# Performance work log

Hardware: AMD Instinct MI355X
Metric: run time of the kernel (lower is better)

## Reference

```python
import jax, jax.numpy as jnp
import numpy as np

DEPTH = 4
EPS = 1e-5


def block_pool(x, g):
    # adaptive max pool over a g x g grid of blocks, broadcast back to full size.
    # Equivalent to the recursive HalfSplit/adaptive_max_pool2d/QuarterStitch pyramid.
    B, C, H, W = x.shape
    xr = x.reshape(B, C, g, H // g, g, W // g)
    m = xr.max(axis=(3, 5), keepdims=True)          # [B,C,g,1,g,1]
    return jnp.broadcast_to(m, xr.shape).reshape(B, C, H, W)


def conv1x1_bn(x, w, gamma, beta):
    # Conv2DNormed: 1x1 conv (no bias) followed by BatchNorm (batch statistics).
    y = jnp.einsum('bchw,oc->bohw', x, w)
    mu = y.mean(axis=(0, 2, 3), keepdims=True)
    var = y.var(axis=(0, 2, 3), keepdims=True)
    yhat = (y - mu) * jax.lax.rsqrt(var + EPS)
    return yhat * gamma[None, :, None, None] + beta[None, :, None, None]


def setup_inputs() -> dict:
    key = jax.random.key(0)
    k0, k1, k2 = jax.random.split(key, 3)
    B, C, H, W = 4, 256, 192, 192
    x = jax.random.normal(k0, (B, C, H, W), jnp.float32)
    ws = jax.random.normal(k1, (DEPTH, C, C), jnp.float32) / np.float32(np.sqrt(C))
    gs = jnp.ones((DEPTH, C), jnp.float32)
    bs = jnp.zeros((DEPTH, C), jnp.float32)
    wf = jax.random.normal(k2, (C, (DEPTH + 1) * C), jnp.float32) / np.float32(np.sqrt((DEPTH + 1) * C))
    gf = jnp.ones((C,), jnp.float32)
    bf = jnp.zeros((C,), jnp.float32)
    return {"x": x, "ws": ws, "gs": gs, "bs": bs, "wf": wf, "gf": gf, "bf": bf}


def reference(x, ws, gs, bs, wf, gf, bf):
    # p[0] = raw input; p[1+d] = conv_d(block-pooled input at grid 2^d), d=0..DEPTH-1
    p = [x]
    for d in range(DEPTH):
        pooled = block_pool(x, 2 ** d)
        p.append(conv1x1_bn(pooled, ws[d], gs[d], bs[d]))
    out = jnp.concatenate(p, axis=1)                # [B, (DEPTH+1)*C, H, W]
    return conv1x1_bn(out, wf, gf, bf)
```

## Files before the change

### kernel.cpp

```cpp
#include <hip/hip_runtime.h>

typedef unsigned short u16;
typedef unsigned int   u32;
typedef __attribute__((ext_vector_type(4))) float f32x4;
typedef __attribute__((ext_vector_type(8))) short s16x8;
typedef __attribute__((ext_vector_type(4))) unsigned short u16x4;

#define HW    36864
#define WPIX  192
#define NCH   256
#define NB    4
#define NPIX  147456
#define POS   85
#define BN_EPS 1e-5f
#define NBKT  16

#define WS_PALL    0
#define WS_YD      (WS_PALL + NB*NCH*POS)
#define WS_PSUM    (WS_YD + NB*NCH*POS)
#define WS_PSQ     (WS_PSUM + 1024)
#define WS_PSC     (WS_PSQ + 1024)
#define WS_PBI     (WS_PSC + 1024)
#define WS_CONTRIB (WS_PBI + 1024)
#define WS_FSUMB   (WS_CONTRIB + NB*NCH*64)
#define WS_FSQB    (WS_FSUMB + NBKT*256)
#define WS_FSC     (WS_FSQB + NBKT*256)
#define WS_FBI     (WS_FSC + 256)
#define WS_WPK     (WS_FBI + 256)
#define WS_YBF     (WS_WPK + 32768)
#define WS_YBF_FLOATS (NB*NCH*HW/2)
#define WS_TOTAL   (WS_YBF + WS_YBF_FLOATS)

__device__ __forceinline__ u16 f2bf(float f) {
  u32 u = __builtin_bit_cast(u32, f);
  u += 0x7fffu + ((u >> 16) & 1u);
  return (u16)(u >> 16);
}
__device__ __forceinline__ float bf2f(u16 h) {
  u32 u = ((u32)h) << 16;
  return __builtin_bit_cast(float, u);
}

__global__ __launch_bounds__(192) void k_pool(const float* __restrict__ x, float* __restrict__ wsb) {
  __shared__ float sm[8][4][48];
  __shared__ float sp[84];
  int bc = blockIdx.x;
  const float* base = x + (size_t)bc * HW;
  int t = threadIdx.x;
  int cg = t % 48, rg = t / 48;
  if (bc == 0) {
    for (int i = t; i < 2048; i += 192) wsb[WS_PSUM + i] = 0.f;
    for (int i = t; i < 2*NBKT*256; i += 192) wsb[WS_FSUMB + i] = 0.f;
  }
  #pragma unroll
  for (int byi = 0; byi < 8; byi++) {
    float mm = -3.4e38f;
    #pragma unroll
    for (int rr = 0; rr < 6; rr++) {
      int r = byi*24 + rg + 4*rr;
      f32x4 v = *(const f32x4*)(base + r*WPIX + cg*4);
      mm = fmaxf(mm, fmaxf(fmaxf(v.x, v.y), fmaxf(v.z, v.w)));
    }
    sm[byi][rg][cg] = mm;
  }
  __syncthreads();
  size_t pb = WS_PALL + (size_t)bc * POS;
  if (t < 64) {
    int by = t >> 3, bx = t & 7;
    float mm = -3.4e38f;
    for (int r2 = 0; r2 < 4; r2++)
      for (int cq = 0; cq < 6; cq++)
        mm = fmaxf(mm, sm[by][r2][bx*6 + cq]);
    sp[t] = mm;
    wsb[pb + t] = mm;
  }
  __syncthreads();
  if (t < 16) {
    int i = t >> 2, j = t & 3;
    float mm = fmaxf(fmaxf(sp[(2*i)*8 + 2*j], sp[(2*i)*8 + 2*j + 1]),
                     fmaxf(sp[(2*i+1)*8 + 2*j], sp[(2*i+1)*8 + 2*j + 1]));
    sp[64 + t] = mm;
    wsb[pb + 64 + t] = mm;
  }
  __syncthreads();
  if (t < 4) {
    int i = t >> 1, j = t & 1;
    float mm = fmaxf(fmaxf(sp[64 + (2*i)*4 + 2*j], sp[64 + (2*i)*4 + 2*j + 1]),
                     fmaxf(sp[64 + (2*i+1)*4 + 2*j], sp[64 + (2*i+1)*4 + 2*j + 1]));
    sp[80 + t] = mm;
    wsb[pb + 80 + t] = mm;
  }
  __syncthreads();
  if (t == 0)
    wsb[pb + 84] = fmaxf(fmaxf(sp[80], sp[81]), fmaxf(sp[82], sp[83]));
}

__global__ __launch_bounds__(256) void k_wpack(const float* __restrict__ wf, float* __restrict__ wsb) {
  int fid = blockIdx.x*256 + threadIdx.x;
  int m = fid & 255, g = (fid >> 8) & 3, ks = fid >> 10;
  const float* src = wf + (size_t)m*1280 + ks*32 + g*8;
  f32x4 a = *(const f32x4*)src;
  f32x4 c = *(const f32x4*)(src + 4);
  u32* dst = (u32*)((u16*)(wsb + WS_WPK) + (size_t)fid*8);
  dst[0] = (u32)f2bf(a.x) | ((u32)f2bf(a.y) << 16);
  dst[1] = (u32)f2bf(a.z) | ((u32)f2bf(a.w) << 16);
  dst[2] = (u32)f2bf(c.x) | ((u32)f2bf(c.y) << 16);
  dst[3] = (u32)f2bf(c.z) | ((u32)f2bf(c.w) << 16);
}

__global__ __launch_bounds__(256) void k_pyr(const float* __restrict__ wconv, float* __restrict__ wsb) {
  __shared__ __align__(16) float pv[256];
  int bi = blockIdx.x;
  int b = bi / 85, pos = bi % 85;
  int d = (pos < 64) ? 3 : (pos < 80) ? 2 : (pos < 84) ? 1 : 0;
  int t = threadIdx.x;
  pv[t] = wsb[WS_PALL + (size_t)(b*NCH + t)*POS + pos];
  __syncthreads();
  const float* wrow = wconv + ((size_t)d*NCH + t)*NCH;
  float acc = 0.f;
  #pragma unroll 4
  for (int c4 = 0; c4 < 64; c4++) {
    f32x4 wv = *(const f32x4*)(wrow + c4*4);
    f32x4 xv = *(const f32x4*)(&pv[c4*4]);
    acc += wv.x*xv.x + wv.y*xv.y + wv.z*xv.z + wv.w*xv.w;
  }
  wsb[WS_YD + (size_t)(b*NCH + t)*POS + pos] = acc;
  atomicAdd(&wsb[WS_PSUM + d*NCH + t], acc);
  atomicAdd(&wsb[WS_PSQ  + d*NCH + t], acc*acc);
}

__global__ void k_pstats(const float* __restrict__ gs, const float* __restrict__ bs, float* __restrict__ wsb) {
  int t = blockIdx.x*256 + threadIdx.x;
  int d = t >> 8;
  float cnt = (float)(4 << (2*d));
  float mu  = wsb[WS_PSUM + t] / cnt;
  float var = wsb[WS_PSQ + t] / cnt - mu*mu;
  float sc  = gs[t] * rsqrtf(var + BN_EPS);
  wsb[WS_PSC + t] = sc;
  wsb[WS_PBI + t] = bs[t] - mu * sc;
}

__global__ __launch_bounds__(256) void k_contrib(const float* __restrict__ wf, float* __restrict__ wsb) {
  __shared__ __align__(16) float pn[1024];
  int bi = blockIdx.x;
  int b = bi >> 6, cell = bi & 63;
  int by = cell >> 3, bx = cell & 7;
  int t = threadIdx.x;
  int pos3 = cell;
  int pos2 = 64 + (by >> 1)*4 + (bx >> 1);
  int pos1 = 80 + (by >> 2)*2 + (bx >> 2);
  size_t yb = WS_YD + (size_t)(b*NCH + t)*POS;
  pn[0*NCH + t] = wsb[yb + 84]   * wsb[WS_PSC + 0*NCH + t] + wsb[WS_PBI + 0*NCH + t];
  pn[1*NCH + t] = wsb[yb + pos1] * wsb[WS_PSC + 1*NCH + t] + wsb[WS_PBI + 1*NCH + t];
  pn[2*NCH + t] = wsb[yb + pos2] * wsb[WS_PSC + 2*NCH + t] + wsb[WS_PBI + 2*NCH + t];
  pn[3*NCH + t] = wsb[yb + pos3] * wsb[WS_PSC + 3*NCH + t] + wsb[WS_PBI + 3*NCH + t];
  __syncthreads();
  const float* wrow = wf + (size_t)t*1280 + 256;
  float acc = 0.f;
  #pragma unroll 4
  for (int j = 0; j < 256; j++) {
    f32x4 wv = *(const f32x4*)(wrow + j*4);
    f32x4 xv = *(const f32x4*)(&pn[j*4]);
    acc += wv.x*xv.x + wv.y*xv.y + wv.z*xv.z + wv.w*xv.w;
  }
  wsb[WS_CONTRIB + (size_t)(b*NCH + t)*64 + cell] = acc;
}

template<bool YBF>
__global__ __launch_bounds__(256) void k_main(const float* __restrict__ x,
                                              float* __restrict__ wsb, float* __restrict__ y) {
  __shared__ __align__(16) u16 xlds[2][64*40];
  int wg = blockIdx.x;
  int b = wg / 576, nt = wg % 576;
  int pbase = nt * 64;
  int by8   = ((nt / 3) / 24) * 8;
  int wbase = (nt % 3) * 64;
  int t = threadIdx.x;
  int wave = t >> 6, l = t & 63;
  int g = l >> 4, ln = l & 15;
  int sn = t & 63;
  int kh = t >> 6;
  const float* xb = x + (size_t)b*NCH*HW + pbase + sn;
  const u16* wpk = (const u16*)(wsb + WS_WPK);
  int mrow = wave*64 + ln;

  f32x4 acc[4][4];
  #pragma unroll
  for (int i = 0; i < 4; i++)
    #pragma unroll
    for (int j = 0; j < 4; j++)
      acc[i][j] = {0.f, 0.f, 0.f, 0.f};

  float xr0[8], xr1[8];
  s16x8 a0[4], a1[4];

  #pragma unroll
  for (int j = 0; j < 8; j++) xr0[j] = xb[(size_t)(kh*8 + j)*HW];
  #pragma unroll
  for (int tm = 0; tm < 4; tm++)
    a0[tm] = *(const s16x8*)(wpk + ((size_t)(0*4 + g)*256 + mrow + tm*16)*8);

  #pragma unroll
  for (int ks = 0; ks < 8; ks++) {
    float    (&xr)[8] = (ks & 1) ? xr1 : xr0;
    s16x8    (&af)[4] = (ks & 1) ? a1  : a0;
    float    (&xrn)[8] = (ks & 1) ? xr0 : xr1;
    s16x8    (&afn)[4] = (ks & 1) ? a0  : a1;
    s16x8 pk;
    #pragma unroll
    for (int j = 0; j < 8; j++) pk[j] = (short)f2bf(xr[j]);
    *(s16x8*)(&xlds[ks & 1][sn*40 + kh*8]) = pk;
    __syncthreads();
    if (ks < 7) {
      #pragma unroll
      for (int j = 0; j < 8; j++) xrn[j] = xb[(size_t)((ks+1)*32 + kh*8 + j)*HW];
      #pragma unroll
      for (int tm = 0; tm < 4; tm++)
        afn[tm] = *(const s16x8*)(wpk + ((size_t)((ks+1)*4 + g)*256 + mrow + tm*16)*8);
    }
    #pragma unroll
    for (int tn = 0; tn < 4; tn++) {
      s16x8 bfr = *(const s16x8*)(&xlds[ks & 1][(tn*16 + ln)*40 + g*8]);
      #pragma unroll
      for (int tm = 0; tm < 4; tm++)
        acc[tm][tn] = __builtin_amdgcn_mfma_f32_16x16x32_bf16(af[tm], bfr, acc[tm][tn], 0, 0, 0);
    }
  }

  const float* cb = wsb + WS_CONTRIB + (size_t)b*NCH*64;
  int bkt = wg & (NBKT - 1);
  float* fsum = wsb + WS_FSUMB + bkt*256;
  float* fsq  = wsb + WS_FSQB  + bkt*256;
  u16*   ybb  = (u16*)(wsb + WS_YBF) + (size_t)b*NCH*HW + pbase;
  float* ybf32 = y + (size_t)b*NCH*HW + pbase;
  #pragma unroll
  for (int tm = 0; tm < 4; tm++) {
    int ob = wave*64 + tm*16 + g*4;
    #pragma unroll
    for (int r = 0; r < 4; r++) {
      int o = ob + r;
      float s1 = 0.f, s2 = 0.f;
      #pragma unroll
      for (int tn = 0; tn < 4; tn++) {
        int n = tn*16 + ln;
        int bx = (wbase + n) / 24;
        float yv = acc[tm][tn][r] + cb[(size_t)o*64 + by8 + bx];
        if (YBF) {
          u16 h = f2bf(yv);
          float yr = bf2f(h);
          ybb[(size_t)o*HW + n] = h;
          s1 += yr; s2 += yr*yr;
        } else {
          ybf32[(size_t)o*HW + n] = yv;
          s1 += yv; s2 += yv*yv;
        }
      }
      s1 += __shfl_xor(s1, 1);  s2 += __shfl_xor(s2, 1);
      s1 += __shfl_xor(s1, 2);  s2 += __shfl_xor(s2, 2);
      s1 += __shfl_xor(s1, 4);  s2 += __shfl_xor(s2, 4);
      s1 += __shfl_xor(s1, 8);  s2 += __shfl_xor(s2, 8);
      if (ln == 0) { atomicAdd(&fsum[o], s1); atomicAdd(&fsq[o], s2); }
    }
  }
}

__global__ void k_fstats(const float* __restrict__ gf, const float* __restrict__ bfv, float* __restrict__ wsb) {
  int o = threadIdx.x;
  float s1 = 0.f, s2 = 0.f;
  #pragma unroll
  for (int i = 0; i < NBKT; i++) {
    s1 += wsb[WS_FSUMB + i*256 + o];
    s2 += wsb[WS_FSQB  + i*256 + o];
  }
  float inv = 1.f / (float)NPIX;
  float mu  = s1 * inv;
  float var = s2 * inv - mu*mu;
  float sc  = gf[o] * rsqrtf(var + BN_EPS);
  wsb[WS_FSC + o] = sc;
  wsb[WS_FBI + o] = bfv[o] - mu * sc;
}

template<bool YBF>
__global__ __launch_bounds__(256) void k_norm(float* __restrict__ out, const float* __restrict__ wsb) {
  int bid = blockIdx.x;
  int plane = bid >> 2, q = bid & 3;
  int c = plane & 255;
  float sc = wsb[WS_FSC + c], bi = wsb[WS_FBI + c];
  size_t base4 = ((size_t)plane*HW + q*(HW/4)) >> 2;
  int t = threadIdx.x;
  if (YBF) {
    const u16* yb = (const u16*)(wsb + WS_YBF);
    #pragma unroll
    for (int it = 0; it < 9; it++) {
      size_t i4 = base4 + it*256 + t;
      u16x4 v = *(const u16x4*)(yb + i4*4);
      f32x4 o;
      o.x = bf2f(v.x)*sc + bi;
      o.y = bf2f(v.y)*sc + bi;
      o.z = bf2f(v.z)*sc + bi;
      o.w = bf2f(v.w)*sc + bi;
      ((f32x4*)out)[i4] = o;
    }
  } else {
    #pragma unroll
    for (int it = 0; it < 9; it++) {
      size_t i4 = base4 + it*256 + t;
      f32x4 v = ((f32x4*)out)[i4];
      v.x = v.x*sc + bi; v.y = v.y*sc + bi; v.z = v.z*sc + bi; v.w = v.w*sc + bi;
      ((f32x4*)out)[i4] = v;
    }
  }
}

extern "C" void kernel_launch(void* const* d_in, const int* in_sizes, int n_in,
                              void* d_out, int out_size, void* d_ws, size_t ws_size,
                              hipStream_t stream) {
  const float* x  = (const float*)d_in[0];
  const float* w  = (const float*)d_in[1];
  const float* gs = (const float*)d_in[2];
  const float* bs = (const float*)d_in[3];
  const float* wf = (const float*)d_in[4];
  const float* gf = (const float*)d_in[5];
  const float* bf = (const float*)d_in[6];
  float* y   = (float*)d_out;
  float* wsb = (float*)d_ws;

  bool ybf = ws_size >= (size_t)WS_TOTAL * sizeof(float);

  k_pool   <<<NB*NCH, 192, 0, stream>>>(x, wsb);
  k_wpack  <<<32, 256, 0, stream>>>(wf, wsb);
  k_pyr    <<<NB*POS, 256, 0, stream>>>(w, wsb);
  k_pstats <<<4, 256, 0, stream>>>(gs, bs, wsb);
  k_contrib<<<NB*64, 256, 0, stream>>>(wf, wsb);
  if (ybf) k_main<true> <<<NB*576, 256, 0, stream>>>(x, wsb, y);
  else     k_main<false><<<NB*576, 256, 0, stream>>>(x, wsb, y);
  k_fstats <<<1, 256, 0, stream>>>(gf, bf, wsb);
  if (ybf) k_norm<true> <<<4096, 256, 0, stream>>>(y, wsb);
  else     k_norm<false><<<4096, 256, 0, stream>>>(y, wsb);
}
```

Before: 200.4 us.

## Pre-transpose input to bf16 pixel-major layout and stream GEMM tiles via global_load_lds

Adds a prep kernel that converts the input once to a bf16 pixel-major, XOR-swizzled layout while computing row maxima, so the main GEMM loads its B tiles straight into LDS with global_load_lds and no per-tile conversion. The main kernel now covers 128 pixels per workgroup, with larger accumulator tiles and a min-blocks launch bound. Small kernels are merged: weight packing goes into prep, pyramid stats are folded into contrib (now split by depth and accumulated with atomics), and final stats are folded into the normalize kernel. The cost is an extra bf16 copy of the input (write then read) and more workspace, which the ybf path now requires.

```diff
diff --git a/kernel.cpp b/kernel.cpp
--- a/kernel.cpp
+++ b/kernel.cpp
@@ -4,10 +4,10 @@
 typedef unsigned int   u32;
 typedef __attribute__((ext_vector_type(4))) float f32x4;
 typedef __attribute__((ext_vector_type(8))) short s16x8;
+typedef __attribute__((ext_vector_type(4))) short s16x4;
 typedef __attribute__((ext_vector_type(4))) unsigned short u16x4;
 
 #define HW    36864
-#define WPIX  192
 #define NCH   256
 #define NB    4
 #define NPIX  147456
@@ -16,20 +16,18 @@
 #define NBKT  16
 
 #define WS_PALL    0
-#define WS_YD      (WS_PALL + NB*NCH*POS)
-#define WS_PSUM    (WS_YD + NB*NCH*POS)
-#define WS_PSQ     (WS_PSUM + 1024)
-#define WS_PSC     (WS_PSQ + 1024)
-#define WS_PBI     (WS_PSC + 1024)
-#define WS_CONTRIB (WS_PBI + 1024)
-#define WS_FSUMB   (WS_CONTRIB + NB*NCH*64)
-#define WS_FSQB    (WS_FSUMB + NBKT*256)
-#define WS_FSC     (WS_FSQB + NBKT*256)
-#define WS_FBI     (WS_FSC + 256)
-#define WS_WPK     (WS_FBI + 256)
-#define WS_YBF     (WS_WPK + 32768)
-#define WS_YBF_FLOATS (NB*NCH*HW/2)
-#define WS_TOTAL   (WS_YBF + WS_YBF_FLOATS)
+#define WS_YD      87040
+#define WS_PSUM    174080
+#define WS_PSQ     175104
+#define WS_CONTRIB 176128
+#define WS_FSUMB   241664
+#define WS_FSQB    245760
+#define WS_RM      249856
+#define WS_WPK     1822720
+#define WS_XT      1855488
+#define WS_YBF     20729856
+#define WS_TOT1    39604224
+#define WS_TOT2    20729856
 
 __device__ __forceinline__ u16 f2bf(float f) {
   u32 u = __builtin_bit_cast(u32, f);
@@ -40,72 +38,122 @@
   u32 u = ((u32)h) << 16;
   return __builtin_bit_cast(float, u);
 }
-
-__global__ __launch_bounds__(192) void k_pool(const float* __restrict__ x, float* __restrict__ wsb) {
-  __shared__ float sm[8][4][48];
-  __shared__ float sp[84];
+__device__ __forceinline__ void gl_lds16(const void* g, void* l) {
+  __builtin_amdgcn_global_load_lds(
+      (const __attribute__((address_space(1))) u32*)g,
+      (__attribute__((address_space(3))) u32*)l, 16, 0, 0);
+}
+
+#define LP 204
+
+__global__ __launch_bounds__(256) void k_prep(const float* __restrict__ x,
+                                              const float* __restrict__ wf,
+                                              float* __restrict__ wsb) {
+  int blk = blockIdx.x;
+  int t = threadIdx.x;
+  if (blk >= 768) {
+    int fid = (blk - 768)*256 + t;
+    int m = fid & 255, g = (fid >> 8) & 3, ks = fid >> 10;
+    const float* src = wf + (size_t)m*1280 + ks*32 + g*8;
+    f32x4 a = *(const f32x4*)src;
+    f32x4 c = *(const f32x4*)(src + 4);
+    u32* dst = (u32*)((u16*)(wsb + WS_WPK) + (size_t)fid*8);
+    dst[0] = (u32)f2bf(a.x) | ((u32)f2bf(a.y) << 16);
+    dst[1] = (u32)f2bf(a.z) | ((u32)f2bf(a.w) << 16);
+    dst[2] = (u32)f2bf(c.x) | ((u32)f2bf(c.y) << 16);
+    dst[3] = (u32)f2bf(c.z) | ((u32)f2bf(c.w) << 16);
+    if (blk == 768) {
+      for (int i = t; i < 2048;  i += 256) wsb[WS_PSUM + i] = 0.f;
+      for (int i = t; i < 65536; i += 256) wsb[WS_CONTRIB + i] = 0.f;
+      for (int i = t; i < 8192;  i += 256) wsb[WS_FSUMB + i] = 0.f;
+    }
+    return;
+  }
+  __shared__ u16 ldsT[32 * LP];
+  int b = blk / 192, r = blk % 192;
+  int c_l = t >> 3, grp = t & 7;
+  int px_w = t >> 2, oct_w = t & 3;
+  u16* xTu = (u16*)(wsb + WS_XT);
+  float* rm = wsb + WS_RM;
+  int p_row = r * 192;
+
+  for (int cc = 0; cc < 8; cc++) {
+    int c = cc*32 + c_l;
+    const float* src = x + (size_t)(b*NCH + c)*HW + p_row + grp*24;
+    float mm = -3.4e38f;
+    #pragma unroll
+    for (int q = 0; q < 6; q++) {
+      f32x4 v = *(const f32x4*)(src + q*4);
+      mm = fmaxf(mm, fmaxf(fmaxf(v.x, v.y), fmaxf(v.z, v.w)));
+      s16x4 pk;
+      pk[0] = (short)f2bf(v.x); pk[1] = (short)f2bf(v.y);
+      pk[2] = (short)f2bf(v.z); pk[3] = (short)f2bf(v.w);
+      *(s16x4*)&ldsT[c_l*LP + grp*24 + q*4] = pk;
+    }
+    rm[((size_t)(b*NCH + c)*192 + r)*8 + grp] = mm;
+    __syncthreads();
+    #pragma unroll
+    for (int i = 0; i < 3; i++) {
+      int px = i*64 + px_w;
+      s16x8 v;
+      #pragma unroll
+      for (int e = 0; e < 8; e++)
+        v[e] = (short)ldsT[(oct_w*8 + e)*LP + px];
+      int p_glob = p_row + px;
+      int slot = oct_w ^ ((px >> 1) & 3);
+      *(s16x8*)(xTu + ((size_t)b*HW + p_glob)*256 + cc*32 + slot*8) = v;
+    }
+    __syncthreads();
+  }
+}
+
+__global__ __launch_bounds__(64) void k_pmax(float* __restrict__ wsb) {
+  __shared__ float sm3[64], sm2[16], sm1[4], arr85[85];
   int bc = blockIdx.x;
-  const float* base = x + (size_t)bc * HW;
-  int t = threadIdx.x;
-  int cg = t % 48, rg = t / 48;
-  if (bc == 0) {
-    for (int i = t; i < 2048; i += 192) wsb[WS_PSUM + i] = 0.f;
-    for (int i = t; i < 2*NBKT*256; i += 192) wsb[WS_FSUMB + i] = 0.f;
-  }
-  #pragma unroll
-  for (int byi = 0; byi < 8; byi++) {
-    float mm = -3.4e38f;
-    #pragma unroll
-    for (int rr = 0; rr < 6; rr++) {
-      int r = byi*24 + rg + 4*rr;
-      f32x4 v = *(const f32x4*)(base + r*WPIX + cg*4);
-      mm = fmaxf(mm, fmaxf(fmaxf(v.x, v.y), fmaxf(v.z, v.w)));
-    }
-    sm[byi][rg][cg] = mm;
-  }
-  __syncthreads();
-  size_t pb = WS_PALL + (size_t)bc * POS;
-  if (t < 64) {
-    int by = t >> 3, bx = t & 7;
-    float mm = -3.4e38f;
-    for (int r2 = 0; r2 < 4; r2++)
-      for (int cq = 0; cq < 6; cq++)
-        mm = fmaxf(mm, sm[by][r2][bx*6 + cq]);
-    sp[t] = mm;
-    wsb[pb + t] = mm;
+  int t = threadIdx.x;
+  const float* rm = wsb + WS_RM + (size_t)bc*1536;
+  float v[24];
+  #pragma unroll
+  for (int q = 0; q < 6; q++)
+    *(f32x4*)&v[q*4] = *(const f32x4*)(rm + t*24 + q*4);
+  float m3p[8];
+  #pragma unroll
+  for (int j = 0; j < 8; j++)
+    m3p[j] = fmaxf(v[j], fmaxf(v[8+j], v[16+j]));
+  #pragma unroll
+  for (int j = 0; j < 8; j++) {
+    float m = m3p[j];
+    m = fmaxf(m, __shfl_xor(m, 1));
+    m = fmaxf(m, __shfl_xor(m, 2));
+    m = fmaxf(m, __shfl_xor(m, 4));
+    m3p[j] = m;
+  }
+  if ((t & 7) == 0) {
+    int br = t >> 3;
+    #pragma unroll
+    for (int j = 0; j < 8; j++) sm3[br*8 + j] = m3p[j];
   }
   __syncthreads();
   if (t < 16) {
     int i = t >> 2, j = t & 3;
-    float mm = fmaxf(fmaxf(sp[(2*i)*8 + 2*j], sp[(2*i)*8 + 2*j + 1]),
-                     fmaxf(sp[(2*i+1)*8 + 2*j], sp[(2*i+1)*8 + 2*j + 1]));
-    sp[64 + t] = mm;
-    wsb[pb + 64 + t] = mm;
+    sm2[t] = fmaxf(fmaxf(sm3[(2*i)*8 + 2*j], sm3[(2*i)*8 + 2*j + 1]),
+                   fmaxf(sm3[(2*i+1)*8 + 2*j], sm3[(2*i+1)*8 + 2*j + 1]));
   }
   __syncthreads();
   if (t < 4) {
     int i = t >> 1, j = t & 1;
-    float mm = fmaxf(fmaxf(sp[64 + (2*i)*4 + 2*j], sp[64 + (2*i)*4 + 2*j + 1]),
-                     fmaxf(sp[64 + (2*i+1)*4 + 2*j], sp[64 + (2*i+1)*4 + 2*j + 1]));
-    sp[80 + t] = mm;
-    wsb[pb + 80 + t] = mm;
-  }
-  __syncthreads();
-  if (t == 0)
-    wsb[pb + 84] = fmaxf(fmaxf(sp[80], sp[81]), fmaxf(sp[82], sp[83]));
-}
-
-__global__ __launch_bounds__(256) void k_wpack(const float* __restrict__ wf, float* __restrict__ wsb) {
-  int fid = blockIdx.x*256 + threadIdx.x;
-  int m = fid & 255, g = (fid >> 8) & 3, ks = fid >> 10;
-  const float* src = wf + (size_t)m*1280 + ks*32 + g*8;
-  f32x4 a = *(const f32x4*)src;
-  f32x4 c = *(const f32x4*)(src + 4);
-  u32* dst = (u32*)((u16*)(wsb + WS_WPK) + (size_t)fid*8);
-  dst[0] = (u32)f2bf(a.x) | ((u32)f2bf(a.y) << 16);
-  dst[1] = (u32)f2bf(a.z) | ((u32)f2bf(a.w) << 16);
-  dst[2] = (u32)f2bf(c.x) | ((u32)f2bf(c.y) << 16);
-  dst[3] = (u32)f2bf(c.z) | ((u32)f2bf(c.w) << 16);
+    sm1[t] = fmaxf(fmaxf(sm2[(2*i)*4 + 2*j], sm2[(2*i)*4 + 2*j + 1]),
+                   fmaxf(sm2[(2*i+1)*4 + 2*j], sm2[(2*i+1)*4 + 2*j + 1]));
+  }
+  __syncthreads();
+  if (t < 64) arr85[t] = sm3[t];
+  if (t < 16) arr85[64 + t] = sm2[t];
+  if (t < 4)  arr85[80 + t] = sm1[t];
+  if (t == 0) arr85[84] = fmaxf(fmaxf(sm1[0], sm1[1]), fmaxf(sm1[2], sm1[3]));
+  __syncthreads();
+  float* pb = wsb + WS_PALL + (size_t)bc*POS;
+  if (t < 85) pb[t] = arr85[t];
+  if (t >= 21 && t < 42) pb[t + 43] = arr85[t + 43];
 }
 
 __global__ __launch_bounds__(256) void k_pyr(const float* __restrict__ wconv, float* __restrict__ wsb) {
@@ -129,98 +177,93 @@
   atomicAdd(&wsb[WS_PSQ  + d*NCH + t], acc*acc);
 }
 
-__global__ void k_pstats(const float* __restrict__ gs, const float* __restrict__ bs, float* __restrict__ wsb) {
-  int t = blockIdx.x*256 + threadIdx.x;
-  int d = t >> 8;
+__global__ __launch_bounds__(256) void k_contrib(const float* __restrict__ wf,
+                                                 const float* __restrict__ gs,
+                                                 const float* __restrict__ bs,
+                                                 float* __restrict__ wsb) {
+  __shared__ __align__(16) float pn[4][256];
+  int bi = blockIdx.x;
+  int d = bi >> 6, cell = bi & 63;
+  int by = cell >> 3, bx = cell & 7;
+  int t = threadIdx.x;
+  int pos = (d == 3) ? cell
+          : (d == 2) ? 64 + (by >> 1)*4 + (bx >> 1)
+          : (d == 1) ? 80 + (by >> 2)*2 + (bx >> 2)
+          : 84;
   float cnt = (float)(4 << (2*d));
-  float mu  = wsb[WS_PSUM + t] / cnt;
-  float var = wsb[WS_PSQ + t] / cnt - mu*mu;
-  float sc  = gs[t] * rsqrtf(var + BN_EPS);
-  wsb[WS_PSC + t] = sc;
-  wsb[WS_PBI + t] = bs[t] - mu * sc;
-}
-
-__global__ __launch_bounds__(256) void k_contrib(const float* __restrict__ wf, float* __restrict__ wsb) {
-  __shared__ __align__(16) float pn[1024];
-  int bi = blockIdx.x;
-  int b = bi >> 6, cell = bi & 63;
-  int by = cell >> 3, bx = cell & 7;
-  int t = threadIdx.x;
-  int pos3 = cell;
-  int pos2 = 64 + (by >> 1)*4 + (bx >> 1);
-  int pos1 = 80 + (by >> 2)*2 + (bx >> 2);
-  size_t yb = WS_YD + (size_t)(b*NCH + t)*POS;
-  pn[0*NCH + t] = wsb[yb + 84]   * wsb[WS_PSC + 0*NCH + t] + wsb[WS_PBI + 0*NCH + t];
-  pn[1*NCH + t] = wsb[yb + pos1] * wsb[WS_PSC + 1*NCH + t] + wsb[WS_PBI + 1*NCH + t];
-  pn[2*NCH + t] = wsb[yb + pos2] * wsb[WS_PSC + 2*NCH + t] + wsb[WS_PBI + 2*NCH + t];
-  pn[3*NCH + t] = wsb[yb + pos3] * wsb[WS_PSC + 3*NCH + t] + wsb[WS_PBI + 3*NCH + t];
-  __syncthreads();
-  const float* wrow = wf + (size_t)t*1280 + 256;
-  float acc = 0.f;
+  float mu  = wsb[WS_PSUM + d*NCH + t] / cnt;
+  float var = wsb[WS_PSQ  + d*NCH + t] / cnt - mu*mu;
+  float sc  = gs[d*NCH + t] * rsqrtf(var + BN_EPS);
+  float bi_ = bs[d*NCH + t] - mu * sc;
+  #pragma unroll
+  for (int b = 0; b < 4; b++)
+    pn[b][t] = wsb[WS_YD + (size_t)(b*NCH + t)*POS + pos] * sc + bi_;
+  __syncthreads();
+  const float* wrow = wf + (size_t)t*1280 + 256 + d*256;
+  float a0 = 0.f, a1 = 0.f, a2 = 0.f, a3 = 0.f;
   #pragma unroll 4
-  for (int j = 0; j < 256; j++) {
+  for (int j = 0; j < 64; j++) {
     f32x4 wv = *(const f32x4*)(wrow + j*4);
-    f32x4 xv = *(const f32x4*)(&pn[j*4]);
-    acc += wv.x*xv.x + wv.y*xv.y + wv.z*xv.z + wv.w*xv.w;
-  }
-  wsb[WS_CONTRIB + (size_t)(b*NCH + t)*64 + cell] = acc;
+    f32x4 p0 = *(const f32x4*)(&pn[0][j*4]);
+    f32x4 p1 = *(const f32x4*)(&pn[1][j*4]);
+    f32x4 p2 = *(const f32x4*)(&pn[2][j*4]);
+    f32x4 p3 = *(const f32x4*)(&pn[3][j*4]);
+    a0 += wv.x*p0.x + wv.y*p0.y + wv.z*p0.z + wv.w*p0.w;
+    a1 += wv.x*p1.x + wv.y*p1.y + wv.z*p1.z + wv.w*p1.w;
+    a2 += wv.x*p2.x + wv.y*p2.y + wv.z*p2.z + wv.w*p2.w;
+    a3 += wv.x*p3.x + wv.y*p3.y + wv.z*p3.z + wv.w*p3.w;
+  }
+  atomicAdd(&wsb[WS_CONTRIB + (size_t)(0*NCH + t)*64 + cell], a0);
+  atomicAdd(&wsb[WS_CONTRIB + (size_t)(1*NCH + t)*64 + cell], a1);
+  atomicAdd(&wsb[WS_CONTRIB + (size_t)(2*NCH + t)*64 + cell], a2);
+  atomicAdd(&wsb[WS_CONTRIB + (size_t)(3*NCH + t)*64 + cell], a3);
 }
 
 template<bool YBF>
-__global__ __launch_bounds__(256) void k_main(const float* __restrict__ x,
-                                              float* __restrict__ wsb, float* __restrict__ y) {
-  __shared__ __align__(16) u16 xlds[2][64*40];
+__global__ __launch_bounds__(256, 3) void k_main(float* __restrict__ wsb, float* __restrict__ y) {
+  __shared__ __align__(16) u16 xlds[2][128*32];
   int wg = blockIdx.x;
-  int b = wg / 576, nt = wg % 576;
-  int pbase = nt * 64;
-  int by8   = ((nt / 3) / 24) * 8;
-  int wbase = (nt % 3) * 64;
+  int b = wg / 288, tile = wg % 288;
+  int n0 = tile * 128;
   int t = threadIdx.x;
   int wave = t >> 6, l = t & 63;
   int g = l >> 4, ln = l & 15;
-  int sn = t & 63;
-  int kh = t >> 6;
-  const float* xb = x + (size_t)b*NCH*HW + pbase + sn;
+  int spix = t >> 2, soct = t & 3;
+  const u16* xT = (const u16*)(wsb + WS_XT) + (size_t)b*HW*256;
   const u16* wpk = (const u16*)(wsb + WS_WPK);
-  int mrow = wave*64 + ln;
-
-  f32x4 acc[4][4];
+
+  f32x4 acc[4][8];
   #pragma unroll
   for (int i = 0; i < 4; i++)
     #pragma unroll
-    for (int j = 0; j < 4; j++)
+    for (int j = 0; j < 8; j++)
       acc[i][j] = {0.f, 0.f, 0.f, 0.f};
 
-  float xr0[8], xr1[8];
-  s16x8 a0[4], a1[4];
-
-  #pragma unroll
-  for (int j = 0; j < 8; j++) xr0[j] = xb[(size_t)(kh*8 + j)*HW];
-  #pragma unroll
-  for (int tm = 0; tm < 4; tm++)
-    a0[tm] = *(const s16x8*)(wpk + ((size_t)(0*4 + g)*256 + mrow + tm*16)*8);
-
+  {
+    const u16* s0 = xT + (size_t)(n0 + spix)*256 + soct*8;
+    gl_lds16(s0, &xlds[0][spix*32 + soct*8]);
+    gl_lds16(s0 + 64*256, &xlds[0][(64 + spix)*32 + soct*8]);
+  }
+
+  s16x8 af[4];
   #pragma unroll
   for (int ks = 0; ks < 8; ks++) {
-    float    (&xr)[8] = (ks & 1) ? xr1 : xr0;
-    s16x8    (&af)[4] = (ks & 1) ? a1  : a0;
-    float    (&xrn)[8] = (ks & 1) ? xr0 : xr1;
-    s16x8    (&afn)[4] = (ks & 1) ? a0  : a1;
-    s16x8 pk;
-    #pragma unroll
-    for (int j = 0; j < 8; j++) pk[j] = (short)f2bf(xr[j]);
-    *(s16x8*)(&xlds[ks & 1][sn*40 + kh*8]) = pk;
+    int abase = (ks*4 + g)*256 + wave*64 + ln;
+    #pragma unroll
+    for (int tm = 0; tm < 4; tm++)
+      af[tm] = *(const s16x8*)(wpk + (size_t)(abase + tm*16)*8);
     __syncthreads();
     if (ks < 7) {
-      #pragma unroll
-      for (int j = 0; j < 8; j++) xrn[j] = xb[(size_t)((ks+1)*32 + kh*8 + j)*HW];
-      #pragma unroll
-      for (int tm = 0; tm < 4; tm++)
-        afn[tm] = *(const s16x8*)(wpk + ((size_t)((ks+1)*4 + g)*256 + mrow + tm*16)*8);
-    }
-    #pragma unroll
-    for (int tn = 0; tn < 4; tn++) {
-      s16x8 bfr = *(const s16x8*)(&xlds[ks & 1][(tn*16 + ln)*40 + g*8]);
+      const u16* s0 = xT + (size_t)(n0 + spix)*256 + (ks + 1)*32 + soct*8;
+      u16* d0 = &xlds[(ks + 1) & 1][spix*32 + soct*8];
+      gl_lds16(s0, d0);
+      gl_lds16(s0 + 64*256, d0 + 64*32);
+    }
+    const u16* xb = xlds[ks & 1];
+    #pragma unroll
+    for (int tn = 0; tn < 8; tn++) {
+      int n = tn*16 + ln;
+      s16x8 bfr = *(const s16x8*)(xb + n*32 + ((g ^ ((n >> 1) & 3))*8));
       #pragma unroll
       for (int tm = 0; tm < 4; tm++)
         acc[tm][tn] = __builtin_amdgcn_mfma_f32_16x16x32_bf16(af[tm], bfr, acc[tm][tn], 0, 0, 0);
@@ -231,27 +274,30 @@
   int bkt = wg & (NBKT - 1);
   float* fsum = wsb + WS_FSUMB + bkt*256;
   float* fsq  = wsb + WS_FSQB  + bkt*256;
-  u16*   ybb  = (u16*)(wsb + WS_YBF) + (size_t)b*NCH*HW + pbase;
-  float* ybf32 = y + (size_t)b*NCH*HW + pbase;
+  u16*   ybb  = (u16*)(wsb + WS_YBF) + (size_t)b*NCH*HW + n0;
+  float* yf   = y + (size_t)b*NCH*HW + n0;
   #pragma unroll
   for (int tm = 0; tm < 4; tm++) {
     int ob = wave*64 + tm*16 + g*4;
     #pragma unroll
-    for (int r = 0; r < 4; r++) {
-      int o = ob + r;
+    for (int r_ = 0; r_ < 4; r_++) {
+      int o = ob + r_;
+      const float* cbo = cb + (size_t)o*64;
       float s1 = 0.f, s2 = 0.f;
       #pragma unroll
-      for (int tn = 0; tn < 4; tn++) {
+      for (int tn = 0; tn < 8; tn++) {
         int n = tn*16 + ln;
-        int bx = (wbase + n) / 24;
-        float yv = acc[tm][tn][r] + cb[(size_t)o*64 + by8 + bx];
+        u32 p = (u32)(n0 + n);
+        u32 row = p / 192u;
+        u32 col = p - row*192u;
+        float yv = acc[tm][tn][r_] + cbo[(row/24u)*8u + col/24u];
         if (YBF) {
           u16 h = f2bf(yv);
           float yr = bf2f(h);
           ybb[(size_t)o*HW + n] = h;
           s1 += yr; s2 += yr*yr;
         } else {
-          ybf32[(size_t)o*HW + n] = yv;
+          yf[(size_t)o*HW + n] = yv;
           s1 += yv; s2 += yv*yv;
         }
       }
@@ -264,28 +310,25 @@
   }
 }
 
-__global__ void k_fstats(const float* __restrict__ gf, const float* __restrict__ bfv, float* __restrict__ wsb) {
-  int o = threadIdx.x;
+template<bool YBF>
+__global__ __launch_bounds__(256) void k_norm(float* __restrict__ out,
+                                              const float* __restrict__ gf,
+                                              const float* __restrict__ bfv,
+                                              const float* __restrict__ wsb) {
+  int bid = blockIdx.x;
+  int plane = bid >> 2, q = bid & 3;
+  int c = plane & 255;
   float s1 = 0.f, s2 = 0.f;
   #pragma unroll
   for (int i = 0; i < NBKT; i++) {
-    s1 += wsb[WS_FSUMB + i*256 + o];
-    s2 += wsb[WS_FSQB  + i*256 + o];
+    s1 += wsb[WS_FSUMB + i*256 + c];
+    s2 += wsb[WS_FSQB  + i*256 + c];
   }
   float inv = 1.f / (float)NPIX;
   float mu  = s1 * inv;
   float var = s2 * inv - mu*mu;
-  float sc  = gf[o] * rsqrtf(var + BN_EPS);
-  wsb[WS_FSC + o] = sc;
-  wsb[WS_FBI + o] = bfv[o] - mu * sc;
-}
-
-template<bool YBF>
-__global__ __launch_bounds__(256) void k_norm(float* __restrict__ out, const float* __restrict__ wsb) {
-  int bid = blockIdx.x;
-  int plane = bid >> 2, q = bid & 3;
-  int c = plane & 255;
-  float sc = wsb[WS_FSC + c], bi = wsb[WS_FBI + c];
+  float sc  = gf[c] * rsqrtf(var + BN_EPS);
+  float bi  = bfv[c] - mu * sc;
   size_t base4 = ((size_t)plane*HW + q*(HW/4)) >> 2;
   int t = threadIdx.x;
   if (YBF) {
@@ -325,16 +368,14 @@
   float* y   = (float*)d_out;
   float* wsb = (float*)d_ws;
 
-  bool ybf = ws_size >= (size_t)WS_TOTAL * sizeof(float);
-
-  k_pool   <<<NB*NCH, 192, 0, stream>>>(x, wsb);
-  k_wpack  <<<32, 256, 0, stream>>>(wf, wsb);
+  bool ybf = ws_size >= (size_t)WS_TOT1 * sizeof(float);
+
+  k_prep   <<<800, 256, 0, stream>>>(x, wf, wsb);
+  k_pmax   <<<NB*NCH, 64, 0, stream>>>(wsb);
   k_pyr    <<<NB*POS, 256, 0, stream>>>(w, wsb);
-  k_pstats <<<4, 256, 0, stream>>>(gs, bs, wsb);
-  k_contrib<<<NB*64, 256, 0, stream>>>(wf, wsb);
-  if (ybf) k_main<true> <<<NB*576, 256, 0, stream>>>(x, wsb, y);
-  else     k_main<false><<<NB*576, 256, 0, stream>>>(x, wsb, y);
-  k_fstats <<<1, 256, 0, stream>>>(gf, bf, wsb);
-  if (ybf) k_norm<true> <<<4096, 256, 0, stream>>>(y, wsb);
-  else     k_norm<false><<<4096, 256, 0, stream>>>(y, wsb);
-}
+  k_contrib<<<256, 256, 0, stream>>>(wf, gs, bs, wsb);
+  if (ybf) k_main<true> <<<NB*288, 256, 0, stream>>>(wsb, y);
+  else     k_main<false><<<NB*288, 256, 0, stream>>>(wsb, y);
+  if (ybf) k_norm<true> <<<4096, 256, 0, stream>>>(y, gf, bf, wsb);
+  else     k_norm<false><<<4096, 256, 0, stream>>>(y, gf, bf, wsb);
+}
```

After: 251.5 us. 1.26x slower.
